# Performance work log

Measured on AMD Instinct MI355X. Metric: run time of the kernel, lower is better.

Reference implementation:

```python
import jax, jax.numpy as jnp
import numpy as np
import math

N_HEADS = 8
Q_DIM = 512          # number of query tokens (first Q_DIM rows of q)
INPUT_DIM = 512
EMBED_DIM = 512
HEAD_DIM = EMBED_DIM // N_HEADS  # key_dim == val_dim == 64
BATCH = 8
TOTAL_TOKENS = 4096  # Q_DIM queries + 3584 context tokens
NORM = 1.0 / math.sqrt(HEAD_DIM)


def setup_inputs() -> dict:
    key = jax.random.key(0)
    k1, k2, k3, k4, k5 = jax.random.split(key, 5)
    stdv = 1.0 / math.sqrt(HEAD_DIM)
    return {
        "q": jax.random.normal(k1, (BATCH, TOTAL_TOKENS, INPUT_DIM), dtype=jnp.float32),
        "W_query": jax.random.uniform(k2, (N_HEADS, INPUT_DIM, HEAD_DIM), minval=-stdv, maxval=stdv, dtype=jnp.float32),
        "W_key": jax.random.uniform(k3, (N_HEADS, INPUT_DIM, HEAD_DIM), minval=-stdv, maxval=stdv, dtype=jnp.float32),
        "W_val": jax.random.uniform(k4, (N_HEADS, INPUT_DIM, HEAD_DIM), minval=-stdv, maxval=stdv, dtype=jnp.float32),
        "W_out": jax.random.uniform(k5, (N_HEADS, HEAD_DIM, EMBED_DIM), minval=-1.0 / math.sqrt(EMBED_DIM), maxval=1.0 / math.sqrt(EMBED_DIM), dtype=jnp.float32),
    }


def reference(q, W_query, W_key, W_val, W_out):
    # Split packed input: first Q_DIM tokens are queries, rest are context.
    q_ = q[:, :Q_DIM, :]          # [b, nq, d_in]
    h = q[:, Q_DIM:, :]           # [b, g, d_in]
    Q = jnp.einsum('bqi,hik->hbqk', q_, W_query)   # [h, b, nq, dk]
    K = jnp.einsum('bgi,hik->hbgk', h, W_key)      # [h, b, g, dk]
    V = jnp.einsum('bgi,hiv->hbgv', h, W_val)      # [h, b, g, dv]
    compat = NORM * jnp.einsum('hbqk,hbgk->hbqg', Q, K)  # [h, b, nq, g]
    attn = jax.nn.softmax(compat, axis=-1)
    heads = jnp.einsum('hbqg,hbgv->hbqv', attn, V)       # [h, b, nq, dv]
    out = jnp.einsum('hbqv,hve->bqe', heads, W_out)      # [b, nq, embed]
    return out
```

## Files before the change

kernel.cpp:

```cpp
#include <hip/hip_runtime.h>

typedef _Float16 f16;
typedef _Float16 f16x4 __attribute__((ext_vector_type(4)));
typedef _Float16 f16x8 __attribute__((ext_vector_type(8)));
typedef float    f32x4 __attribute__((ext_vector_type(4)));

#define MFMA(a,b,c) __builtin_amdgcn_mfma_f32_16x16x32_f16(a,b,c,0,0,0)

#if __has_builtin(__builtin_amdgcn_exp2f)
#define EXP2(x) __builtin_amdgcn_exp2f(x)
#else
#define EXP2(x) exp2f(x)
#endif

__device__ __forceinline__ void gld16(const void* g, void* l) {
  typedef __attribute__((address_space(1))) unsigned GU;
  typedef __attribute__((address_space(3))) unsigned LU;
  __builtin_amdgcn_global_load_lds((GU*)g, (LU*)l, 16, 0, 0);
}

__global__ __launch_bounds__(256) void transp_w(
    const float* __restrict__ Wq, const float* __restrict__ Wk,
    const float* __restrict__ Wv, const float* __restrict__ Wo,
    f16* __restrict__ Wqt, f16* __restrict__ Wkt, f16* __restrict__ Wvt,
    f16* __restrict__ Wot)
{
  __shared__ float T[64 * 65];
  int bid = blockIdx.x, t = threadIdx.x;
  int mat = bid >> 6;
  int i0 = (bid & 7) * 64, c0 = ((bid >> 3) & 7) * 64;
  const float* src; f16* dst; float scale = 1.f;
  if      (mat == 0) { src = Wq; dst = Wqt; scale = 0.125f * 1.4426950408889634f; }
  else if (mat == 1) { src = Wk; dst = Wkt; }
  else if (mat == 2) { src = Wv; dst = Wvt; }
  else               { src = Wo; dst = Wot; }
#pragma unroll
  for (int p = 0; p < 4; ++p) {
    int row = p * 16 + (t >> 4), col = (t & 15) * 4;
    const float* a = (mat < 3)
        ? src + ((c0 >> 6) * 512 + i0 + row) * 64 + col
        : src + (i0 + row) * 512 + c0 + col;
    f32x4 v = *(const f32x4*)a;
    T[row * 65 + col + 0] = v[0] * scale;
    T[row * 65 + col + 1] = v[1] * scale;
    T[row * 65 + col + 2] = v[2] * scale;
    T[row * 65 + col + 3] = v[3] * scale;
  }
  __syncthreads();
#pragma unroll
  for (int p = 0; p < 16; ++p) {
    int cc = (t >> 6) * 16 + p, ii = t & 63;
    dst[(c0 + cc) * 512 + i0 + ii] = (f16)T[ii * 65 + cc];
  }
}

__global__ __launch_bounds__(256) void proj_kernel(
    const float* __restrict__ q,
    const f16* __restrict__ Wqt, const f16* __restrict__ Wkt, const f16* __restrict__ Wvt,
    f16* __restrict__ Qh, f16* __restrict__ Kh, f16* __restrict__ Vtb)
{
  __shared__ f16 Asl[2][4096];
  __shared__ f16 Bsl[2][4096];

  int bid = blockIdx.x;
  int mode, t;
  if (bid < 128)       { mode = 0; t = bid; }
  else if (bid < 1024) { mode = 1; t = bid - 128; }
  else                 { mode = 2; t = bid - 1024; }
  int rt = t >> 2, ct = t & 3;
  const f16* Wt = (mode == 0) ? Wqt : (mode == 1) ? Wkt : Wvt;

  int tid = threadIdx.x, l = tid & 63, w = tid >> 6;
  int m0 = rt * 128, n0 = ct * 128;
  int wr = w >> 1, wc = w & 1;

  int arl = tid >> 3;
  int acol = (tid & 7) * 4;
  int agrow[4], awb[4];
#pragma unroll
  for (int p = 0; p < 4; ++p) {
    int m = m0 + p * 32 + arl;
    int grow;
    if (mode == 0) grow = (m >> 9) * 4096 + (m & 511);
    else { int b = m / 3584; grow = b * 4096 + 512 + (m - b * 3584); }
    agrow[p] = grow * 512;
    int r = p * 32 + arl, cg = tid & 7;
    awb[p] = r * 64 + (((cg >> 1) ^ (r & 3)) << 4) + (cg & 1) * 8;
  }
  int bn[2], bco[2];
#pragma unroll
  for (int j = 0; j < 2; ++j) {
    int n = (w * 2 + j) * 16 + (l >> 2);
    bn[j] = n;
    bco[j] = ((l & 3) ^ (n & 3)) * 8;
  }

  const f32x4 z4 = {0.f, 0.f, 0.f, 0.f};
  f32x4 acc[4][4];
#pragma unroll
  for (int i = 0; i < 4; ++i)
#pragma unroll
    for (int jj = 0; jj < 4; ++jj) acc[i][jj] = z4;

  f32x4 areg[4];
  auto aload = [&](int k0) {
#pragma unroll
    for (int p = 0; p < 4; ++p)
      areg[p] = *(const f32x4*)(q + agrow[p] + k0 + acol);
  };
  auto bstage = [&](int bufi, int k0) {
#pragma unroll
    for (int j = 0; j < 2; ++j)
      gld16(Wt + (n0 + bn[j]) * 512 + k0 + bco[j], &Bsl[bufi][(w * 2 + j) * 512]);
  };
  auto awrite = [&](int bufi) {
#pragma unroll
    for (int p = 0; p < 4; ++p) {
      f16x4 h4;
      h4[0] = (f16)areg[p][0]; h4[1] = (f16)areg[p][1];
      h4[2] = (f16)areg[p][2]; h4[3] = (f16)areg[p][3];
      *(f16x4*)((char*)&Asl[bufi][0] + awb[p]) = h4;
    }
  };

  aload(0); bstage(0, 0); awrite(0);
  __syncthreads();

  for (int ks = 0; ks < 16; ++ks) {
    int bufi = ks & 1;
    if (ks < 15) { aload((ks + 1) * 32); bstage(bufi ^ 1, (ks + 1) * 32); }
    const char* AB = (const char*)&Asl[bufi][0];
    const char* BB = (const char*)&Bsl[bufi][0];
    f16x8 af[4], bf[4];
#pragma unroll
    for (int mi = 0; mi < 4; ++mi) {
      int row = wr * 64 + mi * 16 + (l & 15);
      af[mi] = *(const f16x8*)(AB + row * 64 + (((l >> 4) ^ (row & 3)) << 4));
    }
#pragma unroll
    for (int ni = 0; ni < 4; ++ni) {
      int rn = wc * 64 + ni * 16 + (l & 15);
      bf[ni] = *(const f16x8*)(BB + rn * 64 + (((l >> 4) ^ (rn & 3)) << 4));
    }
#pragma unroll
    for (int mi = 0; mi < 4; ++mi)
#pragma unroll
      for (int ni = 0; ni < 4; ++ni)
        acc[mi][ni] = MFMA(af[mi], bf[ni], acc[mi][ni]);
    if (ks < 15) awrite(bufi ^ 1);
    __syncthreads();
  }

  if (mode < 2) {
    f16* Out = (mode == 0) ? Qh : Kh;
#pragma unroll
    for (int mi = 0; mi < 4; ++mi) {
      int row = m0 + wr * 64 + mi * 16 + (l >> 4) * 4;
#pragma unroll
      for (int ni = 0; ni < 4; ++ni) {
        int col = n0 + wc * 64 + ni * 16 + (l & 15);
#pragma unroll
        for (int r = 0; r < 4; ++r)
          Out[(row + r) * 512 + col] = (f16)acc[mi][ni][r];
      }
    }
  } else {
#pragma unroll
    for (int mi = 0; mi < 4; ++mi) {
      int m = m0 + wr * 64 + mi * 16 + (l >> 4) * 4;
      int b = m / 3584, g = m - b * 3584;
#pragma unroll
      for (int ni = 0; ni < 4; ++ni) {
        int c = n0 + wc * 64 + ni * 16 + (l & 15);
        int hh = c >> 6, v = c & 63;
        f16x4 o4;
        o4[0] = (f16)acc[mi][ni][0]; o4[1] = (f16)acc[mi][ni][1];
        o4[2] = (f16)acc[mi][ni][2]; o4[3] = (f16)acc[mi][ni][3];
        *(f16x4*)(Vtb + ((b * 8 + hh) * 64 + v) * 3584 + g) = o4;
      }
    }
  }
}

__global__ __launch_bounds__(512, 4) void attn_kernel(
    const f16* __restrict__ Qh, const f16* __restrict__ Kh,
    const f16* __restrict__ Vtb, f16* __restrict__ Opart,
    float* __restrict__ Ml, float* __restrict__ Ll)
{
  __shared__ f16 Klds[2][4096];
  __shared__ f16 Vlds[2][4096];
  __shared__ f16 Plds[8 * 1152];

  int bid = blockIdx.x;
  int seg = bid & 1, qt = (bid >> 1) & 3, h = (bid >> 3) & 7, bb = bid >> 6;
  int q0 = qt * 128;
  int tid = threadIdx.x, l = tid & 63, w = tid >> 6;

  f16x8 qf0, qf1;
  {
    int qrow = q0 + w * 16 + (l & 15);
    const f16* qb = Qh + (bb * 512 + qrow) * 512 + h * 64 + ((l >> 4) * 8);
    qf0 = *(const f16x8*)qb;
    qf1 = *(const f16x8*)(qb + 32);
  }

  bool isK = (w < 4);
  int sdo[2], ssrc[2];
#pragma unroll
  for (int j = 0; j < 2; ++j) {
    int id = (isK ? w : (w - 4)) * 2 + j;
    int rr = id * 8 + (l >> 3);
    int co = ((l & 7) ^ (rr & 7)) * 8;
    sdo[j] = id * 512;
    if (isK) ssrc[j] = (bb * 3584 + seg * 1792 + rr) * 512 + h * 64 + co;
    else     ssrc[j] = ((bb * 8 + h) * 64 + rr) * 3584 + seg * 1792 + co;
  }

  const f32x4 z4 = {0.f, 0.f, 0.f, 0.f};
  f32x4 acco[4];
#pragma unroll
  for (int i = 0; i < 4; ++i) acco[i] = z4;
  float mrow = -1e30f, lrow = 0.f;

  char* PwB = (char*)&Plds[w * 1152];
  int pwbase = (l & 15) * 144 + (l >> 4) * 8;
  int prbase = (l & 15) * 144 + (l >> 4) * 16;

  if (isK) { gld16(Kh + ssrc[0], &Klds[0][sdo[0]]); gld16(Kh + ssrc[1], &Klds[0][sdo[1]]); }
  else     { gld16(Vtb + ssrc[0], &Vlds[0][sdo[0]]); gld16(Vtb + ssrc[1], &Vlds[0][sdo[1]]); }
  __syncthreads();

  int buf = 0;
  for (int it = 0; it < 28; ++it) {
    if (it < 27) {
      int g0 = (it + 1) * 64;
      if (isK) { gld16(Kh + ssrc[0] + g0 * 512, &Klds[buf ^ 1][sdo[0]]);
                 gld16(Kh + ssrc[1] + g0 * 512, &Klds[buf ^ 1][sdo[1]]); }
      else     { gld16(Vtb + ssrc[0] + g0, &Vlds[buf ^ 1][sdo[0]]);
                 gld16(Vtb + ssrc[1] + g0, &Vlds[buf ^ 1][sdo[1]]); }
    }
    const char* KB = (const char*)&Klds[buf][0];
    const char* VB = (const char*)&Vlds[buf][0];

    f32x4 accs[4];
#pragma unroll
    for (int i = 0; i < 4; ++i) accs[i] = z4;
#pragma unroll
    for (int ni = 0; ni < 4; ++ni) {
      int g = ni * 16 + (l & 15);
      const char* rp = KB + g * 128;
      f16x8 k0 = *(const f16x8*)(rp + ((((l >> 4)    ) ^ (g & 7)) << 4));
      f16x8 k1 = *(const f16x8*)(rp + (((4 + (l >> 4)) ^ (g & 7)) << 4));
      accs[ni] = MFMA(k0, qf0, accs[ni]);
      accs[ni] = MFMA(k1, qf1, accs[ni]);
    }

    float n0 = fmaxf(fmaxf(accs[0][0], accs[0][1]), fmaxf(accs[0][2], accs[0][3]));
    float n1 = fmaxf(fmaxf(accs[1][0], accs[1][1]), fmaxf(accs[1][2], accs[1][3]));
    float n2 = fmaxf(fmaxf(accs[2][0], accs[2][1]), fmaxf(accs[2][2], accs[2][3]));
    float n3 = fmaxf(fmaxf(accs[3][0], accs[3][1]), fmaxf(accs[3][2], accs[3][3]));
    float tm = fmaxf(fmaxf(n0, n1), fmaxf(n2, n3));
    tm = fmaxf(tm, __shfl_xor(tm, 16));
    tm = fmaxf(tm, __shfl_xor(tm, 32));
    float mn = fmaxf(mrow, tm);
    float alpha = EXP2(mrow - mn);
    mrow = mn;

    float rs = 0.f;
#pragma unroll
    for (int ni = 0; ni < 4; ++ni) {
      float s0 = EXP2(accs[ni][0] - mrow);
      float s1 = EXP2(accs[ni][1] - mrow);
      float s2 = EXP2(accs[ni][2] - mrow);
      float s3 = EXP2(accs[ni][3] - mrow);
      rs += (s0 + s1) + (s2 + s3);
      f16x4 p4;
      p4[0] = (f16)s0; p4[1] = (f16)s1; p4[2] = (f16)s2; p4[3] = (f16)s3;
      *(f16x4*)(PwB + pwbase + ni * 32) = p4;
    }
    rs += __shfl_xor(rs, 16);
    rs += __shfl_xor(rs, 32);
    lrow = lrow * alpha + rs;
#pragma unroll
    for (int ni = 0; ni < 4; ++ni)
#pragma unroll
      for (int r = 0; r < 4; ++r) acco[ni][r] *= alpha;

    asm volatile("s_waitcnt lgkmcnt(0)" ::: "memory");

#pragma unroll
    for (int kc = 0; kc < 2; ++kc) {
      f16x8 pf = *(const f16x8*)(PwB + prbase + kc * 64);
#pragma unroll
      for (int ni = 0; ni < 4; ++ni) {
        int v = ni * 16 + (l & 15);
        f16x8 vf = *(const f16x8*)(VB + v * 128 + (((kc * 4 + (l >> 4)) ^ (v & 7)) << 4));
        acco[ni] = MFMA(vf, pf, acco[ni]);
      }
    }

    __syncthreads();
    buf ^= 1;
  }

  float inv = 1.f / lrow;
  int q = q0 + w * 16 + (l & 15);
  size_t obase = ((size_t)(seg * 64 + bb * 8 + h) * 512 + q) * 64;
#pragma unroll
  for (int ni = 0; ni < 4; ++ni) {
    f16x4 o4;
    o4[0] = (f16)(acco[ni][0] * inv); o4[1] = (f16)(acco[ni][1] * inv);
    o4[2] = (f16)(acco[ni][2] * inv); o4[3] = (f16)(acco[ni][3] * inv);
    *(f16x4*)(Opart + obase + ni * 16 + (l >> 4) * 4) = o4;
  }
  if ((l >> 4) == 0) {
    int mi = (seg * 64 + bb * 8 + h) * 512 + q;
    Ml[mi] = mrow; Ll[mi] = lrow;
  }
}

__global__ __launch_bounds__(256) void merge_kernel(
    const f16* __restrict__ Opart, const float* __restrict__ Ml,
    const float* __restrict__ Ll, f16* __restrict__ Hm)
{
  int row = blockIdx.x * 4 + (threadIdx.x >> 6);
  int l = threadIdx.x & 63;
  int bh = row >> 9, q = row & 511;
  int i0 = bh * 512 + q;
  int i1 = (64 + bh) * 512 + q;
  float o0 = (float)Opart[(size_t)i0 * 64 + l];
  float o1 = (float)Opart[(size_t)i1 * 64 + l];
  float m0 = Ml[i0], l0 = Ll[i0], m1 = Ml[i1], l1 = Ll[i1];
  float m = fmaxf(m0, m1);
  float w0 = EXP2(m0 - m) * l0, w1 = EXP2(m1 - m) * l1;
  float o = (w0 * o0 + w1 * o1) / (w0 + w1);
  int bb = bh >> 3, hh = bh & 7;
  Hm[((size_t)(bb * 512 + q)) * 512 + hh * 64 + l] = (f16)o;
}

__global__ __launch_bounds__(256) void outproj_kernel(
    const f16* __restrict__ Hm, const f16* __restrict__ Wot, float* __restrict__ out)
{
  __shared__ f16 Asl[2][4096];
  __shared__ f16 Bsl[2][4096];
  int bid = blockIdx.x;
  int rt = bid >> 2, ct = bid & 3;
  int tid = threadIdx.x, l = tid & 63, w = tid >> 6;
  int m0 = rt * 128, n0 = ct * 128;
  int wr = w >> 1, wc = w & 1;

  int an[2], aco[2];
#pragma unroll
  for (int j = 0; j < 2; ++j) {
    int r = (w * 2 + j) * 16 + (l >> 2);
    an[j] = r;
    aco[j] = ((l & 3) ^ (r & 3)) * 8;
  }

  const f32x4 z4 = {0.f, 0.f, 0.f, 0.f};
  f32x4 acc[4][4];
#pragma unroll
  for (int i = 0; i < 4; ++i)
#pragma unroll
    for (int jj = 0; jj < 4; ++jj) acc[i][jj] = z4;

  auto stage = [&](int bufi, int k0) {
#pragma unroll
    for (int j = 0; j < 2; ++j) {
      gld16(Hm  + (m0 + an[j]) * 512 + k0 + aco[j], &Asl[bufi][(w * 2 + j) * 512]);
      gld16(Wot + (n0 + an[j]) * 512 + k0 + aco[j], &Bsl[bufi][(w * 2 + j) * 512]);
    }
  };

  stage(0, 0);
  __syncthreads();
  for (int ks = 0; ks < 16; ++ks) {
    int bufi = ks & 1;
    if (ks < 15) stage(bufi ^ 1, (ks + 1) * 32);
    const char* AB = (const char*)&Asl[bufi][0];
    const char* BB = (const char*)&Bsl[bufi][0];
    f16x8 af[4], bf[4];
#pragma unroll
    for (int mi = 0; mi < 4; ++mi) {
      int row = wr * 64 + mi * 16 + (l & 15);
      af[mi] = *(const f16x8*)(AB + row * 64 + (((l >> 4) ^ (row & 3)) << 4));
    }
#pragma unroll
    for (int ni = 0; ni < 4; ++ni) {
      int rn = wc * 64 + ni * 16 + (l & 15);
      bf[ni] = *(const f16x8*)(BB + rn * 64 + (((l >> 4) ^ (rn & 3)) << 4));
    }
#pragma unroll
    for (int mi = 0; mi < 4; ++mi)
#pragma unroll
      for (int ni = 0; ni < 4; ++ni)
        acc[mi][ni] = MFMA(af[mi], bf[ni], acc[mi][ni]);
    __syncthreads();
  }

#pragma unroll
  for (int mi = 0; mi < 4; ++mi) {
    int row = m0 + wr * 64 + mi * 16 + (l >> 4) * 4;
#pragma unroll
    for (int ni = 0; ni < 4; ++ni) {
      int col = n0 + wc * 64 + ni * 16 + (l & 15);
#pragma unroll
      for (int r = 0; r < 4; ++r)
        out[(row + r) * 512 + col] = acc[mi][ni][r];
    }
  }
}

extern "C" void kernel_launch(void* const* d_in, const int* in_sizes, int n_in,
                              void* d_out, int out_size, void* d_ws, size_t ws_size,
                              hipStream_t stream) {
  const float* q  = (const float*)d_in[0];
  const float* Wq = (const float*)d_in[1];
  const float* Wk = (const float*)d_in[2];
  const float* Wv = (const float*)d_in[3];
  const float* Wo = (const float*)d_in[4];
  float* out = (float*)d_out;

  f16* ws  = (f16*)d_ws;
  f16* Wqt = ws;
  f16* Wkt = Wqt + 262144;
  f16* Wvt = Wkt + 262144;
  f16* Wot = Wvt + 262144;
  f16* Qh  = Wot + 262144;
  f16* Kh  = Qh  + 4096 * 512;
  f16* Vtb = Kh  + 28672 * 512;
  f16* Opart = Vtb + 28672 * 512;
  float* Ml = (float*)(Opart + 2 * 64 * 512 * 64);
  float* Ll = Ml + 65536;
  f16* Hm = Qh;

  transp_w<<<dim3(256),  dim3(256), 0, stream>>>(Wq, Wk, Wv, Wo, Wqt, Wkt, Wvt, Wot);
  proj_kernel<<<dim3(1920), dim3(256), 0, stream>>>(q, Wqt, Wkt, Wvt, Qh, Kh, Vtb);
  attn_kernel<<<dim3(512), dim3(512), 0, stream>>>(Qh, Kh, Vtb, Opart, Ml, Ll);
  merge_kernel<<<dim3(8192), dim3(256), 0, stream>>>(Opart, Ml, Ll, Hm);
  outproj_kernel<<<dim3(128), dim3(256), 0, stream>>>(Hm, Wot, out);
}
```

Before: 243.1 us.

## Restructure projection GEMM so each block covers all output columns and fuses K/V

The projection kernel is reorganized so each 512-thread block computes every output column for its row tile. For context rows, K and V are computed together from one shared A tile, so the fp32 input rows are loaded and converted once instead of eight times (four column tiles each for K and V). Weight fragments now come straight from global memory into registers with double buffering, and the B tile in LDS is removed. This cuts redundant reads of the large activation input but raises register pressure (128 accumulator floats per thread) and puts the weight loads on global/L2 latency.

```diff
diff --git a/kernel.cpp b/kernel.cpp
--- a/kernel.cpp
+++ b/kernel.cpp
@@ -54,129 +54,139 @@
   }
 }
 
-__global__ __launch_bounds__(256) void proj_kernel(
+__global__ __launch_bounds__(512, 2) void proj_kernel(
     const float* __restrict__ q,
     const f16* __restrict__ Wqt, const f16* __restrict__ Wkt, const f16* __restrict__ Wvt,
     f16* __restrict__ Qh, f16* __restrict__ Kh, f16* __restrict__ Vtb)
 {
   __shared__ f16 Asl[2][4096];
-  __shared__ f16 Bsl[2][4096];
-
-  int bid = blockIdx.x;
-  int mode, t;
-  if (bid < 128)       { mode = 0; t = bid; }
-  else if (bid < 1024) { mode = 1; t = bid - 128; }
-  else                 { mode = 2; t = bid - 1024; }
-  int rt = t >> 2, ct = t & 3;
-  const f16* Wt = (mode == 0) ? Wqt : (mode == 1) ? Wkt : Wvt;
-
-  int tid = threadIdx.x, l = tid & 63, w = tid >> 6;
-  int m0 = rt * 128, n0 = ct * 128;
-  int wr = w >> 1, wc = w & 1;
-
-  int arl = tid >> 3;
-  int acol = (tid & 7) * 4;
-  int agrow[4], awb[4];
-#pragma unroll
-  for (int p = 0; p < 4; ++p) {
-    int m = m0 + p * 32 + arl;
-    int grow;
-    if (mode == 0) grow = (m >> 9) * 4096 + (m & 511);
-    else { int b = m / 3584; grow = b * 4096 + 512 + (m - b * 3584); }
-    agrow[p] = grow * 512;
-    int r = p * 32 + arl, cg = tid & 7;
-    awb[p] = r * 64 + (((cg >> 1) ^ (r & 3)) << 4) + (cg & 1) * 8;
-  }
-  int bn[2], bco[2];
-#pragma unroll
-  for (int j = 0; j < 2; ++j) {
-    int n = (w * 2 + j) * 16 + (l >> 2);
-    bn[j] = n;
-    bco[j] = ((l & 3) ^ (n & 3)) * 8;
+
+  int bid = blockIdx.x, tid = threadIdx.x, l = tid & 63, w = tid >> 6;
+  bool qmode = bid < 32;
+
+  int srow = tid >> 3, colg = tid & 7;
+  int chunk = colg >> 1, sub = colg & 1;
+  const float *ap0, *ap1 = nullptr;
+  if (qmode) {
+    int m = bid * 128 + srow;
+    ap0 = q + ((size_t)((m >> 9) * 4096 + (m & 511))) * 512 + colg * 4;
+    int m2 = m + 64;
+    ap1 = q + ((size_t)((m2 >> 9) * 4096 + (m2 & 511))) * 512 + colg * 4;
+  } else {
+    int m = (bid - 32) * 64 + srow;
+    int b = m / 3584;
+    ap0 = q + ((size_t)(b * 4096 + 512 + (m - b * 3584))) * 512 + colg * 4;
+  }
+  int wo0 = chunk * 2048 + ((srow * 16 + chunk * 32) & 2047) + sub * 8;
+  int wo1 = chunk * 2048 + (((srow + 64) * 16 + chunk * 32) & 2047) + sub * 8;
+
+  const f16* Wt;
+  int wrow;
+  if (qmode) { Wt = Wqt; wrow = (w >> 2) * 64; }
+  else       { Wt = (w < 4) ? Wkt : Wvt; wrow = 0; }
+  int colbase = (w & 3) * 128;
+  const f16* bbase = Wt + (size_t)(colbase + (l & 15)) * 512 + (l >> 4) * 8;
+
+  int ro[4];
+#pragma unroll
+  for (int mi = 0; mi < 4; ++mi) {
+    int row = wrow + mi * 16 + (l & 15);
+    ro[mi] = (l >> 4) * 2048 + ((row * 16 + (l >> 4) * 32) & 2047);
   }
 
   const f32x4 z4 = {0.f, 0.f, 0.f, 0.f};
-  f32x4 acc[4][4];
+  f32x4 acc[4][8];
 #pragma unroll
   for (int i = 0; i < 4; ++i)
 #pragma unroll
-    for (int jj = 0; jj < 4; ++jj) acc[i][jj] = z4;
-
-  f32x4 areg[4];
-  auto aload = [&](int k0) {
-#pragma unroll
-    for (int p = 0; p < 4; ++p)
-      areg[p] = *(const f32x4*)(q + agrow[p] + k0 + acol);
+    for (int j = 0; j < 8; ++j) acc[i][j] = z4;
+
+  f16x8 bfr[2][8];
+  f32x4 ar0, ar1;
+
+  auto awrite = [&](int bufi) {
+    f16x4 h4;
+    h4[0] = (f16)ar0[0]; h4[1] = (f16)ar0[1]; h4[2] = (f16)ar0[2]; h4[3] = (f16)ar0[3];
+    *(f16x4*)((char*)&Asl[bufi][0] + wo0) = h4;
+    if (qmode) {
+      f16x4 g4;
+      g4[0] = (f16)ar1[0]; g4[1] = (f16)ar1[1]; g4[2] = (f16)ar1[2]; g4[3] = (f16)ar1[3];
+      *(f16x4*)((char*)&Asl[bufi][0] + wo1) = g4;
+    }
   };
-  auto bstage = [&](int bufi, int k0) {
-#pragma unroll
-    for (int j = 0; j < 2; ++j)
-      gld16(Wt + (n0 + bn[j]) * 512 + k0 + bco[j], &Bsl[bufi][(w * 2 + j) * 512]);
-  };
-  auto awrite = [&](int bufi) {
-#pragma unroll
-    for (int p = 0; p < 4; ++p) {
-      f16x4 h4;
-      h4[0] = (f16)areg[p][0]; h4[1] = (f16)areg[p][1];
-      h4[2] = (f16)areg[p][2]; h4[3] = (f16)areg[p][3];
-      *(f16x4*)((char*)&Asl[bufi][0] + awb[p]) = h4;
-    }
-  };
-
-  aload(0); bstage(0, 0); awrite(0);
+
+  ar0 = *(const f32x4*)ap0;
+  if (qmode) ar1 = *(const f32x4*)ap1;
+#pragma unroll
+  for (int ni = 0; ni < 8; ++ni)
+    bfr[0][ni] = *(const f16x8*)(bbase + ni * 8192);
+  awrite(0);
   __syncthreads();
 
+#pragma unroll
   for (int ks = 0; ks < 16; ++ks) {
-    int bufi = ks & 1;
-    if (ks < 15) { aload((ks + 1) * 32); bstage(bufi ^ 1, (ks + 1) * 32); }
-    const char* AB = (const char*)&Asl[bufi][0];
-    const char* BB = (const char*)&Bsl[bufi][0];
-    f16x8 af[4], bf[4];
+    int cur = ks & 1;
+    f16x8 af[4];
+#pragma unroll
+    for (int mi = 0; mi < 4; ++mi)
+      af[mi] = *(const f16x8*)((const char*)&Asl[cur][0] + ro[mi]);
+    if (ks < 15) {
+      int k0 = (ks + 1) * 32;
+      ar0 = *(const f32x4*)(ap0 + k0);
+      if (qmode) ar1 = *(const f32x4*)(ap1 + k0);
+#pragma unroll
+      for (int ni = 0; ni < 8; ++ni)
+        bfr[cur ^ 1][ni] = *(const f16x8*)(bbase + ni * 8192 + k0);
+    }
+#pragma unroll
+    for (int mi = 0; mi < 4; ++mi)
+#pragma unroll
+      for (int ni = 0; ni < 8; ++ni)
+        acc[mi][ni] = MFMA(af[mi], bfr[cur][ni], acc[mi][ni]);
+    if (ks < 15) awrite(cur ^ 1);
+    __syncthreads();
+  }
+
+  if (qmode) {
+    int rowb = bid * 128 + (w >> 2) * 64;
 #pragma unroll
     for (int mi = 0; mi < 4; ++mi) {
-      int row = wr * 64 + mi * 16 + (l & 15);
-      af[mi] = *(const f16x8*)(AB + row * 64 + (((l >> 4) ^ (row & 3)) << 4));
-    }
-#pragma unroll
-    for (int ni = 0; ni < 4; ++ni) {
-      int rn = wc * 64 + ni * 16 + (l & 15);
-      bf[ni] = *(const f16x8*)(BB + rn * 64 + (((l >> 4) ^ (rn & 3)) << 4));
-    }
-#pragma unroll
-    for (int mi = 0; mi < 4; ++mi)
-#pragma unroll
-      for (int ni = 0; ni < 4; ++ni)
-        acc[mi][ni] = MFMA(af[mi], bf[ni], acc[mi][ni]);
-    if (ks < 15) awrite(bufi ^ 1);
-    __syncthreads();
-  }
-
-  if (mode < 2) {
-    f16* Out = (mode == 0) ? Qh : Kh;
+      int row = rowb + mi * 16 + (l >> 4) * 4;
+#pragma unroll
+      for (int ni = 0; ni < 8; ++ni) {
+        int col = colbase + ni * 16 + (l & 15);
+#pragma unroll
+        for (int r = 0; r < 4; ++r)
+          Qh[(size_t)(row + r) * 512 + col] = (f16)acc[mi][ni][r];
+      }
+    }
+  } else if (w < 4) {
+    int rowb = (bid - 32) * 64;
 #pragma unroll
     for (int mi = 0; mi < 4; ++mi) {
-      int row = m0 + wr * 64 + mi * 16 + (l >> 4) * 4;
-#pragma unroll
-      for (int ni = 0; ni < 4; ++ni) {
-        int col = n0 + wc * 64 + ni * 16 + (l & 15);
+      int row = rowb + mi * 16 + (l >> 4) * 4;
+#pragma unroll
+      for (int ni = 0; ni < 8; ++ni) {
+        int col = colbase + ni * 16 + (l & 15);
 #pragma unroll
         for (int r = 0; r < 4; ++r)
-          Out[(row + r) * 512 + col] = (f16)acc[mi][ni][r];
+          Kh[(size_t)(row + r) * 512 + col] = (f16)acc[mi][ni][r];
       }
     }
   } else {
+    int m0v = (bid - 32) * 64;
+    int b = m0v / 3584, g0 = m0v - b * 3584;
 #pragma unroll
     for (int mi = 0; mi < 4; ++mi) {
-      int m = m0 + wr * 64 + mi * 16 + (l >> 4) * 4;
-      int b = m / 3584, g = m - b * 3584;
-#pragma unroll
-      for (int ni = 0; ni < 4; ++ni) {
-        int c = n0 + wc * 64 + ni * 16 + (l & 15);
+      int g = g0 + mi * 16 + (l >> 4) * 4;
+#pragma unroll
+      for (int ni = 0; ni < 8; ++ni) {
+        int c = colbase + ni * 16 + (l & 15);
         int hh = c >> 6, v = c & 63;
         f16x4 o4;
         o4[0] = (f16)acc[mi][ni][0]; o4[1] = (f16)acc[mi][ni][1];
         o4[2] = (f16)acc[mi][ni][2]; o4[3] = (f16)acc[mi][ni][3];
-        *(f16x4*)(Vtb + ((b * 8 + hh) * 64 + v) * 3584 + g) = o4;
+        *(f16x4*)(Vtb + (size_t)((b * 8 + hh) * 64 + v) * 3584 + g) = o4;
       }
     }
   }
@@ -435,7 +445,7 @@
   f16* Hm = Qh;
 
   transp_w<<<dim3(256),  dim3(256), 0, stream>>>(Wq, Wk, Wv, Wo, Wqt, Wkt, Wvt, Wot);
-  proj_kernel<<<dim3(1920), dim3(256), 0, stream>>>(q, Wqt, Wkt, Wvt, Qh, Kh, Vtb);
+  proj_kernel<<<dim3(480), dim3(512), 0, stream>>>(q, Wqt, Wkt, Wvt, Qh, Kh, Vtb);
   attn_kernel<<<dim3(512), dim3(512), 0, stream>>>(Qh, Kh, Vtb, Opart, Ml, Ll);
   merge_kernel<<<dim3(8192), dim3(256), 0, stream>>>(Opart, Ml, Ll, Hm);
   outproj_kernel<<<dim3(128), dim3(256), 0, stream>>>(Hm, Wot, out);
```

New measurement: 242.5 us. No clear change (-0.2%).

## Remap projection tiles for cache locality and vectorize A/B staging loads

Applied to the files above, without the earlier changes.

The projection GEMM gets a new block-to-tile mapping. It interleaves K and V column tiles of the same row tile and spreads tiles across XCDs with a stride-8 mapping, so that a block's q rows and weights are reused from L2. The A staging now loads 16 contiguous floats per thread and writes 16-byte LDS stores. B is loaded as full rows with a new XOR swizzle. A launch-bounds occupancy hint of 3 is added. The risks are register pressure under the hint and correctness of the new swizzle and tile mapping.

```diff
diff --git a/kernel.cpp b/kernel.cpp
--- a/kernel.cpp
+++ b/kernel.cpp
@@ -54,7 +54,7 @@
   }
 }
 
-__global__ __launch_bounds__(256) void proj_kernel(
+__global__ __launch_bounds__(256, 3) void proj_kernel(
     const float* __restrict__ q,
     const f16* __restrict__ Wqt, const f16* __restrict__ Wkt, const f16* __restrict__ Wvt,
     f16* __restrict__ Qh, f16* __restrict__ Kh, f16* __restrict__ Vtb)
@@ -62,37 +62,50 @@
   __shared__ f16 Asl[2][4096];
   __shared__ f16 Bsl[2][4096];
 
-  int bid = blockIdx.x;
-  int mode, t;
-  if (bid < 128)       { mode = 0; t = bid; }
-  else if (bid < 1024) { mode = 1; t = bid - 128; }
-  else                 { mode = 2; t = bid - 1024; }
-  int rt = t >> 2, ct = t & 3;
-  const f16* Wt = (mode == 0) ? Wqt : (mode == 1) ? Wkt : Wvt;
+  int bid0 = blockIdx.x;
+  int tile = (bid0 & 7) * 240 + (bid0 >> 3);
 
   int tid = threadIdx.x, l = tid & 63, w = tid >> 6;
-  int m0 = rt * 128, n0 = ct * 128;
   int wr = w >> 1, wc = w & 1;
 
-  int arl = tid >> 3;
-  int acol = (tid & 7) * 4;
-  int agrow[4], awb[4];
-#pragma unroll
-  for (int p = 0; p < 4; ++p) {
-    int m = m0 + p * 32 + arl;
-    int grow;
-    if (mode == 0) grow = (m >> 9) * 4096 + (m & 511);
-    else { int b = m / 3584; grow = b * 4096 + 512 + (m - b * 3584); }
-    agrow[p] = grow * 512;
-    int r = p * 32 + arl, cg = tid & 7;
-    awb[p] = r * 64 + (((cg >> 1) ^ (r & 3)) << 4) + (cg & 1) * 8;
-  }
-  int bn[2], bco[2];
+  bool qmode = tile < 128;
+  int rt, colbase, vmode = 0;
+  const f16* Wt;
+  if (qmode) {
+    rt = tile >> 2; colbase = (tile & 3) * 128; Wt = Wqt;
+  } else {
+    int t2 = tile - 128; rt = t2 >> 3; int cc = t2 & 7;
+    if (cc < 4) { Wt = Wkt; colbase = cc * 128; }
+    else        { Wt = Wvt; colbase = (cc - 4) * 128; vmode = 1; }
+  }
+  int gbase, bidx;
+  if (qmode) { bidx = rt >> 2; gbase = bidx * 4096 + (rt & 3) * 128; }
+  else       { bidx = rt / 28; gbase = bidx * 4096 + 512 + (rt * 128 - bidx * 3584); }
+
+  const float* asrc[2];
+  const f16*   bsrc[2];
+  int ldst[2];
 #pragma unroll
   for (int j = 0; j < 2; ++j) {
-    int n = (w * 2 + j) * 16 + (l >> 2);
-    bn[j] = n;
-    bco[j] = ((l & 3) ^ (n & 3)) * 8;
+    int s = tid + j * 256;
+    int r = s >> 2;
+    int c = (s & 3) ^ ((r >> 1) & 3);
+    asrc[j] = q  + (size_t)(gbase + r) * 512 + c * 8;
+    bsrc[j] = Wt + (size_t)(colbase + r) * 512 + c * 8;
+    ldst[j] = (j * 256 + w * 64) * 8;
+  }
+  int awrow = tid >> 1, awh = tid & 1;
+  int awo0 = awrow * 64 + (((awh * 2 + 0) ^ ((awrow >> 1) & 3)) << 4);
+  int awo1 = awrow * 64 + (((awh * 2 + 1) ^ ((awrow >> 1) & 3)) << 4);
+  const float* awsrc = q + (size_t)(gbase + awrow) * 512 + awh * 16;
+
+  int aro[4], bro[4];
+#pragma unroll
+  for (int i = 0; i < 4; ++i) {
+    int ra = wr * 64 + i * 16 + (l & 15);
+    aro[i] = ra * 64 + ((((l >> 4)) ^ ((ra >> 1) & 3)) << 4);
+    int rb = wc * 64 + i * 16 + (l & 15);
+    bro[i] = rb * 64 + ((((l >> 4)) ^ ((rb >> 1) & 3)) << 4);
   }
 
   const f32x4 z4 = {0.f, 0.f, 0.f, 0.f};
@@ -100,83 +113,97 @@
 #pragma unroll
   for (int i = 0; i < 4; ++i)
 #pragma unroll
-    for (int jj = 0; jj < 4; ++jj) acc[i][jj] = z4;
-
-  f32x4 areg[4];
-  auto aload = [&](int k0) {
-#pragma unroll
-    for (int p = 0; p < 4; ++p)
-      areg[p] = *(const f32x4*)(q + agrow[p] + k0 + acol);
-  };
-  auto bstage = [&](int bufi, int k0) {
-#pragma unroll
-    for (int j = 0; j < 2; ++j)
-      gld16(Wt + (n0 + bn[j]) * 512 + k0 + bco[j], &Bsl[bufi][(w * 2 + j) * 512]);
-  };
-  auto awrite = [&](int bufi) {
-#pragma unroll
-    for (int p = 0; p < 4; ++p) {
-      f16x4 h4;
-      h4[0] = (f16)areg[p][0]; h4[1] = (f16)areg[p][1];
-      h4[2] = (f16)areg[p][2]; h4[3] = (f16)areg[p][3];
-      *(f16x4*)((char*)&Asl[bufi][0] + awb[p]) = h4;
-    }
-  };
-
-  aload(0); bstage(0, 0); awrite(0);
+    for (int j = 0; j < 4; ++j) acc[i][j] = z4;
+
+  f32x4 ar0, ar1, ar2, ar3;
+
+  ar0 = *(const f32x4*)(awsrc + 0);
+  ar1 = *(const f32x4*)(awsrc + 4);
+  ar2 = *(const f32x4*)(awsrc + 8);
+  ar3 = *(const f32x4*)(awsrc + 12);
+  gld16(bsrc[0], &Bsl[0][ldst[0]]);
+  gld16(bsrc[1], &Bsl[0][ldst[1]]);
+  {
+    f16x8 h0, h1;
+#pragma unroll
+    for (int e = 0; e < 4; ++e) { h0[e] = (f16)ar0[e]; h0[4+e] = (f16)ar1[e];
+                                  h1[e] = (f16)ar2[e]; h1[4+e] = (f16)ar3[e]; }
+    *(f16x8*)((char*)&Asl[0][0] + awo0) = h0;
+    *(f16x8*)((char*)&Asl[0][0] + awo1) = h1;
+  }
   __syncthreads();
 
   for (int ks = 0; ks < 16; ++ks) {
-    int bufi = ks & 1;
-    if (ks < 15) { aload((ks + 1) * 32); bstage(bufi ^ 1, (ks + 1) * 32); }
-    const char* AB = (const char*)&Asl[bufi][0];
-    const char* BB = (const char*)&Bsl[bufi][0];
+    int cur = ks & 1;
+    if (ks < 15) {
+      int k0 = (ks + 1) * 32;
+      ar0 = *(const f32x4*)(awsrc + k0 + 0);
+      ar1 = *(const f32x4*)(awsrc + k0 + 4);
+      ar2 = *(const f32x4*)(awsrc + k0 + 8);
+      ar3 = *(const f32x4*)(awsrc + k0 + 12);
+      gld16(bsrc[0] + k0, &Bsl[cur ^ 1][ldst[0]]);
+      gld16(bsrc[1] + k0, &Bsl[cur ^ 1][ldst[1]]);
+    }
+    const char* AB = (const char*)&Asl[cur][0];
+    const char* BB = (const char*)&Bsl[cur][0];
     f16x8 af[4], bf[4];
 #pragma unroll
-    for (int mi = 0; mi < 4; ++mi) {
-      int row = wr * 64 + mi * 16 + (l & 15);
-      af[mi] = *(const f16x8*)(AB + row * 64 + (((l >> 4) ^ (row & 3)) << 4));
-    }
-#pragma unroll
-    for (int ni = 0; ni < 4; ++ni) {
-      int rn = wc * 64 + ni * 16 + (l & 15);
-      bf[ni] = *(const f16x8*)(BB + rn * 64 + (((l >> 4) ^ (rn & 3)) << 4));
-    }
+    for (int i = 0; i < 4; ++i) af[i] = *(const f16x8*)(AB + aro[i]);
+#pragma unroll
+    for (int i = 0; i < 4; ++i) bf[i] = *(const f16x8*)(BB + bro[i]);
 #pragma unroll
     for (int mi = 0; mi < 4; ++mi)
 #pragma unroll
       for (int ni = 0; ni < 4; ++ni)
         acc[mi][ni] = MFMA(af[mi], bf[ni], acc[mi][ni]);
-    if (ks < 15) awrite(bufi ^ 1);
+    if (ks < 15) {
+      f16x8 h0, h1;
+#pragma unroll
+      for (int e = 0; e < 4; ++e) { h0[e] = (f16)ar0[e]; h0[4+e] = (f16)ar1[e];
+                                    h1[e] = (f16)ar2[e]; h1[4+e] = (f16)ar3[e]; }
+      *(f16x8*)((char*)&Asl[cur ^ 1][0] + awo0) = h0;
+      *(f16x8*)((char*)&Asl[cur ^ 1][0] + awo1) = h1;
+    }
     __syncthreads();
   }
 
-  if (mode < 2) {
-    f16* Out = (mode == 0) ? Qh : Kh;
+  if (qmode) {
 #pragma unroll
     for (int mi = 0; mi < 4; ++mi) {
-      int row = m0 + wr * 64 + mi * 16 + (l >> 4) * 4;
+      int row = rt * 128 + wr * 64 + mi * 16 + (l >> 4) * 4;
 #pragma unroll
       for (int ni = 0; ni < 4; ++ni) {
-        int col = n0 + wc * 64 + ni * 16 + (l & 15);
+        int col = colbase + wc * 64 + ni * 16 + (l & 15);
 #pragma unroll
         for (int r = 0; r < 4; ++r)
-          Out[(row + r) * 512 + col] = (f16)acc[mi][ni][r];
+          Qh[(size_t)(row + r) * 512 + col] = (f16)acc[mi][ni][r];
       }
     }
+  } else if (!vmode) {
+#pragma unroll
+    for (int mi = 0; mi < 4; ++mi) {
+      int row = rt * 128 + wr * 64 + mi * 16 + (l >> 4) * 4;
+#pragma unroll
+      for (int ni = 0; ni < 4; ++ni) {
+        int col = colbase + wc * 64 + ni * 16 + (l & 15);
+#pragma unroll
+        for (int r = 0; r < 4; ++r)
+          Kh[(size_t)(row + r) * 512 + col] = (f16)acc[mi][ni][r];
+      }
+    }
   } else {
+    int g0 = rt * 128 - bidx * 3584;
 #pragma unroll
     for (int mi = 0; mi < 4; ++mi) {
-      int m = m0 + wr * 64 + mi * 16 + (l >> 4) * 4;
-      int b = m / 3584, g = m - b * 3584;
+      int g = g0 + wr * 64 + mi * 16 + (l >> 4) * 4;
 #pragma unroll
       for (int ni = 0; ni < 4; ++ni) {
-        int c = n0 + wc * 64 + ni * 16 + (l & 15);
-        int hh = c >> 6, v = c & 63;
+        int c4 = colbase + wc * 64 + ni * 16 + (l & 15);
+        int hh = c4 >> 6, v = c4 & 63;
         f16x4 o4;
         o4[0] = (f16)acc[mi][ni][0]; o4[1] = (f16)acc[mi][ni][1];
         o4[2] = (f16)acc[mi][ni][2]; o4[3] = (f16)acc[mi][ni][3];
-        *(f16x4*)(Vtb + ((b * 8 + hh) * 64 + v) * 3584 + g) = o4;
+        *(f16x4*)(Vtb + (size_t)((bidx * 8 + hh) * 64 + v) * 3584 + g) = o4;
       }
     }
   }
```

Result: faster. 231.6 us (-4.7%).
